# Kernel tuning notes

Measured on AMD Instinct MI355X. Metric: run time of the kernel, lower is better.

Reference implementation:

```python
import jax, jax.numpy as jnp
import numpy as np

EPS = 1e-5
KS = 3  # deformable kernel size
K2 = KS * KS


def conv2d(x, w, stride=1, padding=1):
    return jax.lax.conv_general_dilated(
        x, w, window_strides=(stride, stride),
        padding=[(padding, padding), (padding, padding)],
        dimension_numbers=("NCHW", "OIHW", "NCHW"))


def batchnorm(x, gamma, beta):
    # training-mode BN: batch statistics over (N, H, W)
    mean = jnp.mean(x, axis=(0, 2, 3), keepdims=True)
    var = jnp.var(x, axis=(0, 2, 3), keepdims=True)
    xhat = (x - mean) * jax.lax.rsqrt(var + EPS)
    return xhat * gamma[None, :, None, None] + beta[None, :, None, None]


def deform_conv(x, offsets, w, pad=1):
    # x: (B,C,H,W); offsets: (B,2*K2,H,W) -> first K2 channels = row (y)
    # offsets, next K2 = col (x) offsets; w: (O,C,KS,KS)
    B, C, H, W = x.shape
    xp = jnp.pad(x, ((0, 0), (0, 0), (pad, pad), (pad, pad)))
    Hp, Wp = H + 2 * pad, W + 2 * pad
    # base grid (center of each output pixel in padded coords)
    p0_y = jnp.arange(H, dtype=x.dtype) + pad            # (H,)
    p0_x = jnp.arange(W, dtype=x.dtype) + pad            # (W,)
    # kernel tap offsets in [-1, 0, 1]^2, row-major
    pn = jnp.stack(jnp.meshgrid(jnp.arange(KS) - pad, jnp.arange(KS) - pad,
                                indexing="ij"), axis=-1).reshape(K2, 2).astype(x.dtype)
    off = offsets.reshape(B, 2, K2, H, W)
    off_y = jnp.transpose(off[:, 0], (0, 2, 3, 1))       # (B,H,W,K2)
    off_x = jnp.transpose(off[:, 1], (0, 2, 3, 1))
    py = p0_y[None, :, None, None] + pn[:, 0][None, None, None, :] + off_y
    px = p0_x[None, None, :, None] + pn[:, 1][None, None, None, :] + off_x
    py = jnp.clip(py, 0.0, Hp - 1.0)
    px = jnp.clip(px, 0.0, Wp - 1.0)
    y0 = jnp.floor(py).astype(jnp.int32)
    x0 = jnp.floor(px).astype(jnp.int32)
    y1 = jnp.minimum(y0 + 1, Hp - 1)
    x1 = jnp.minimum(x0 + 1, Wp - 1)
    wy = (py - y0.astype(x.dtype))[:, None]              # (B,1,H,W,K2)
    wx = (px - x0.astype(x.dtype))[:, None]

    def gather(xb, yi, xi):                              # xb (C,Hp,Wp)
        return xb[:, yi, xi]                             # (C,H,W,K2)
    g = jax.vmap(gather)
    v00 = g(xp, y0, x0)
    v01 = g(xp, y0, x1)
    v10 = g(xp, y1, x0)
    v11 = g(xp, y1, x1)
    sampled = (v00 * (1 - wy) * (1 - wx) + v01 * (1 - wy) * wx +
               v10 * wy * (1 - wx) + v11 * wy * wx)      # (B,C,H,W,K2)
    return jnp.einsum("bchwk,ock->bohw", sampled, w.reshape(w.shape[0], C, K2))


def setup_inputs() -> dict:
    key = jax.random.key(0)
    ks = jax.random.split(key, 16)
    B, Cin, P, H, W = 64, 64, 64, 64, 64
    s = lambda k, shp, fan: jax.random.normal(k, shp, jnp.float32) * (fan ** -0.5)
    return {
        "x": jax.random.normal(ks[0], (B, Cin, H, W), jnp.float32),
        "conv1_w": s(ks[1], (P, Cin, 3, 3), Cin * 9),
        "bn1_g": jnp.ones((P,), jnp.float32), "bn1_b": jnp.zeros((P,), jnp.float32),
        "conv2_w": s(ks[2], (16, P, 1, 1), P),
        "bn2_g": jnp.ones((16,), jnp.float32), "bn2_b": jnp.zeros((16,), jnp.float32),
        "off_w": s(ks[3], (18, 16, 3, 3), 16 * 9) * 0.1,
        "off_b": jnp.zeros((18,), jnp.float32),
        "conv3_w": s(ks[4], (16, 16, 3, 3), 16 * 9),
        "bn3_g": jnp.ones((16,), jnp.float32), "bn3_b": jnp.zeros((16,), jnp.float32),
        "conv4_w": s(ks[5], (P, 16, 3, 3), 16 * 9),
        "bn4_g": jnp.ones((P,), jnp.float32), "bn4_b": jnp.zeros((P,), jnp.float32),
    }


def reference(x, conv1_w, bn1_g, bn1_b, conv2_w, bn2_g, bn2_b, off_w, off_b,
              conv3_w, bn3_g, bn3_b, conv4_w, bn4_g, bn4_b):
    out = jax.nn.relu(batchnorm(conv2d(x, conv1_w, 1, 1), bn1_g, bn1_b))
    out = jax.nn.relu(batchnorm(conv2d(out, conv2_w, 1, 0), bn2_g, bn2_b))
    offsets = conv2d(out, off_w, 1, 1) + off_b[None, :, None, None]
    out = jax.nn.relu(batchnorm(deform_conv(out, offsets, conv3_w), bn3_g, bn3_b))
    out = batchnorm(conv2d(out, conv4_w, 1, 1), bn4_g, bn4_b)
    out = out + x  # identity shortcut (stride=1, in_planes==planes)
    return jax.nn.relu(out)
```

## Files before the change

### kernel.cpp

```cpp
#include <hip/hip_runtime.h>

#define BN_N 262144.0f

typedef unsigned short u16;
typedef __attribute__((ext_vector_type(8))) short short8;
typedef __attribute__((ext_vector_type(4))) float floatx4;

#define RP1 4224
#define IS1 278784
#define RP2 1584
#define IS2 104544
#define H2P_TOTAL 6690816

static __device__ __forceinline__ u16 f2bf(float f) {
  union { float f; unsigned u; } v; v.f = f;
  unsigned u = v.u;
  return (u16)((u + 0x7FFFu + ((u >> 16) & 1u)) >> 16);
}
static __device__ __forceinline__ float bf2f(u16 h) {
  union { unsigned u; float f; } v; v.u = ((unsigned)h) << 16;
  return v.f;
}
static __device__ __forceinline__ void cp16(const u16* g, u16* l) {
  __builtin_amdgcn_global_load_lds((const __attribute__((address_space(1))) unsigned int*)g,
                                   (__attribute__((address_space(3))) unsigned int*)l, 16, 0, 0);
}

__global__ __launch_bounds__(256) void prep_weights_k(const float* __restrict__ w1,
                                                      const float* __restrict__ w4,
                                                      const float* __restrict__ w3,
                                                      const float* __restrict__ ow,
                                                      u16* __restrict__ Bsw, u16* __restrict__ Bsw4,
                                                      u16* __restrict__ Bsw3, u16* __restrict__ BswO) {
  int blk = blockIdx.x, tid = threadIdx.x;
  if (blk < 144) {
    int d = blk * 256 + tid;
    int kin = d & 7, n = (d >> 3) & 63, kgrp = (d >> 9) & 3, kc = d >> 11;
    int k = kc * 32 + kgrp * 8 + kin;
    int tap = k >> 6, c = k & 63;
    Bsw[d] = f2bf(w1[n * 576 + c * 9 + tap]);
  } else if (blk < 184) {
    int d = (blk - 144) * 256 + tid;
    int kin = d & 7, n = (d >> 3) & 63, lkk = (d >> 9) & 3, kk = d >> 11;
    int tap = kk * 2 + (lkk >> 1);
    int c = ((lkk & 1) << 3) + kin;
    float v = (tap < 9) ? w4[n * 144 + c * 9 + tap] : 0.f;
    Bsw4[d] = f2bf(v);
  } else if (blk < 194) {
    int d = (blk - 184) * 256 + tid;
    int kin = d & 7, n = (d >> 3) & 15, lkk = (d >> 7) & 3, kk = d >> 9;
    int k = kk * 32 + lkk * 8 + kin;
    int tap = k >> 4, c = k & 15;
    float v = (tap < 9) ? w3[n * 144 + c * 9 + tap] : 0.f;
    Bsw3[d] = f2bf(v);
  } else {
    int d = (blk - 194) * 256 + tid;
    int kin = d & 7, n = (d >> 3) & 31, lkk = (d >> 8) & 3, kk = d >> 10;
    int tap = kk * 2 + (lkk >> 1);
    int c = ((lkk & 1) << 3) + kin;
    float v = (tap < 9 && n < 18) ? ow[n * 144 + c * 9 + tap] : 0.f;
    BswO[d] = f2bf(v);
  }
}

__global__ __launch_bounds__(256) void prep_x_k(const float* __restrict__ x,
                                                u16* __restrict__ xp) {
  int yp = blockIdx.x;
  int b = blockIdx.y;
  int tid = threadIdx.x;
  u16* rowbase = xp + (size_t)(b * 66 + yp) * RP1;
  if (yp == 0 || yp == 65) {
    for (int i = tid; i < RP1 / 4; i += 256)
      ((ushort4*)rowbase)[i] = make_ushort4(0, 0, 0, 0);
    return;
  }
  int y = yp - 1;
  __shared__ __align__(16) u16 s[64][72];
  for (int i = tid; i < 4096; i += 256) {
    int c = i >> 6, xx = i & 63;
    s[xx][c] = f2bf(x[((b * 64 + c) << 12) + (y << 6) + xx]);
  }
  if (tid < 128) {
    int c = tid & 63;
    int pxp = (tid >> 6) ? 65 : 0;
    rowbase[pxp * 64 + c] = 0;
  }
  __syncthreads();
  for (int j = tid; j < 512; j += 256) {
    int xx = j >> 3, chunk = j & 7;
    int pxp = xx + 1;
    int ph = chunk ^ (pxp & 7);
    *(short8*)(rowbase + pxp * 64 + ph * 8) = *(const short8*)(&s[xx][chunk * 8]);
  }
}

__global__ __launch_bounds__(512, 2) void conv1_mfma(const u16* __restrict__ xp,
                                                     const u16* __restrict__ Bsw,
                                                     u16* __restrict__ h1,
                                                     float* __restrict__ sum1, float* __restrict__ sq1) {
  __shared__ __align__(16) u16 ring[43520];
  __shared__ float LS[256], LQ[256];
  const int tid = threadIdx.x;
  const int w8 = tid >> 6, l = tid & 63;
  const int r = w8 & 3, g = w8 >> 2;
  const int lm = l & 15, lk = l >> 4;
  const int b = blockIdx.x >> 2;
  const int quarter = blockIdx.x & 3;
  const int c0 = quarter * 8;
  const u16* xb = xp + (size_t)b * 66 * RP1;

  short8 bReg[18][2];
#pragma unroll
  for (int kk = 0; kk < 18; ++kk)
#pragma unroll
    for (int j = 0; j < 2; ++j)
      bReg[kk][j] = *(const short8*)(Bsw + (((kk * 4 + lk) * 64) + (g * 2 + j) * 16 + lm) * 8);

#pragma unroll
  for (int c = 0; c < 3; ++c) {
    const u16* src = xb + (size_t)(2 * (c0 + c)) * RP1;
    u16* dst = ring + ((c0 + c) % 5) * 8704;
    for (int s = w8; s < 17; s += 8) cp16(src + s * 512 + l * 8, dst + s * 512);
  }
  asm volatile("s_waitcnt vmcnt(0)" ::: "memory");
  __builtin_amdgcn_s_barrier();
  __builtin_amdgcn_sched_barrier(0);

  float ssum[2] = {0.f, 0.f}, sqsm[2] = {0.f, 0.f};

#pragma unroll 1
  for (int j = 0; j < 4; ++j) {
    const int y0 = quarter * 16 + j * 4;
    if (j < 3) {
#pragma unroll
      for (int c = 0; c < 2; ++c) {
        const int ch = c0 + 2 * j + 3 + c;
        const u16* src = xb + (size_t)(2 * ch) * RP1;
        u16* dst = ring + (ch % 5) * 8704;
        for (int s = w8; s < 17; s += 8) cp16(src + s * 512 + l * 8, dst + s * 512);
      }
      __builtin_amdgcn_sched_barrier(0);
    }

    floatx4 acc[4][2];
#pragma unroll
    for (int mt = 0; mt < 4; ++mt)
#pragma unroll
      for (int nb = 0; nb < 2; ++nb)
        acc[mt][nb] = (floatx4){0.f, 0.f, 0.f, 0.f};

#pragma unroll
    for (int kk = 0; kk < 18; ++kk) {
      const int tap = kk >> 1;
      const int dy = (tap < 3) ? 0 : ((tap < 6) ? 1 : 2);
      const int dx = tap - dy * 3;
      const int chunk16 = ((kk & 1) << 2) + lk;
      const int pr = y0 + r + dy;
      const u16* abase = ring + ((pr >> 1) % 5) * 8704 + (pr & 1) * 4224;
      short8 aF[4];
#pragma unroll
      for (int mt = 0; mt < 4; ++mt) {
        int pxp = mt * 16 + lm + dx;
        int ph = chunk16 ^ (pxp & 7);
        aF[mt] = *(const short8*)(abase + pxp * 64 + ph * 8);
      }
#pragma unroll
      for (int mt = 0; mt < 4; ++mt)
#pragma unroll
        for (int nb = 0; nb < 2; ++nb)
          acc[mt][nb] = __builtin_amdgcn_mfma_f32_16x16x32_bf16(aF[mt], bReg[kk][nb], acc[mt][nb], 0, 0, 0);
    }

    const int y = y0 + r;
#pragma unroll
    for (int mt = 0; mt < 4; ++mt)
#pragma unroll
      for (int nb = 0; nb < 2; ++nb) {
        const int oc = g * 32 + nb * 16 + lm;
        u16* dst = h1 + ((size_t)(b * 64 + oc) << 12) + (y << 6) + mt * 16 + (lk << 2);
        floatx4 v = acc[mt][nb];
        *(ushort4*)dst = make_ushort4(f2bf(v.x), f2bf(v.y), f2bf(v.z), f2bf(v.w));
      }

#pragma unroll
    for (int nb = 0; nb < 2; ++nb)
#pragma unroll
      for (int mt = 0; mt < 4; ++mt) {
        floatx4 a = acc[mt][nb];
        ssum[nb] += a.x + a.y + a.z + a.w;
        sqsm[nb] += a.x * a.x + a.y * a.y + a.z * a.z + a.w * a.w;
      }

    if (j < 3) {
      asm volatile("s_waitcnt vmcnt(8)" ::: "memory");
      __builtin_amdgcn_s_barrier();
      __builtin_amdgcn_sched_barrier(0);
    }
  }

#pragma unroll
  for (int nb = 0; nb < 2; ++nb) {
    ssum[nb] += __shfl_xor(ssum[nb], 16, 64);  ssum[nb] += __shfl_xor(ssum[nb], 32, 64);
    sqsm[nb] += __shfl_xor(sqsm[nb], 16, 64);  sqsm[nb] += __shfl_xor(sqsm[nb], 32, 64);
  }
  if (lk == 0) {
#pragma unroll
    for (int nb = 0; nb < 2; ++nb) {
      const int oc = g * 32 + nb * 16 + lm;
      LS[r * 64 + oc] = ssum[nb];  LQ[r * 64 + oc] = sqsm[nb];
    }
  }
  __syncthreads();
  if (tid < 64) atomicAdd(&sum1[tid], LS[tid] + LS[64 + tid] + LS[128 + tid] + LS[192 + tid]);
  else if (tid < 128) { int o = tid - 64; atomicAdd(&sq1[o], LQ[o] + LQ[64 + o] + LQ[128 + o] + LQ[192 + o]); }
}

__global__ __launch_bounds__(256) void conv2_k(const u16* __restrict__ h1,
                                               const float* __restrict__ w2,
                                               const float* __restrict__ sum1, const float* __restrict__ sq1,
                                               const float* __restrict__ g1, const float* __restrict__ b1,
                                               float* __restrict__ out,
                                               float* __restrict__ sum2, float* __restrict__ sq2) {
  __shared__ float s_wt[64 * 16];
  __shared__ float s_scale[64], s_shift[64];
  __shared__ float ls[4][16], lsq[4][16];
  int tid = threadIdx.x;
  for (int i = tid; i < 1024; i += 256) {
    int o = i >> 6, c = i & 63;
    s_wt[c * 16 + o] = w2[i];
  }
  if (tid < 64) {
    float m = sum1[tid] / BN_N;
    float var = sq1[tid] / BN_N - m * m;
    float sc = g1[tid] * rsqrtf(var + 1e-5f);
    s_scale[tid] = sc;
    s_shift[tid] = b1[tid] - m * sc;
  }
  __syncthreads();
  int p = blockIdx.x * 256 + tid;
  int b = p >> 12, r = p & 4095;
  const u16* src = h1 + ((size_t)b << 18) + r;
  float acc[16];
#pragma unroll
  for (int o = 0; o < 16; ++o) acc[o] = 0.f;
  for (int c = 0; c < 64; ++c) {
    float v = bf2f(src[c << 12]);
    v = fmaxf(v * s_scale[c] + s_shift[c], 0.f);
    const float* wp = &s_wt[c * 16];
    float4 w0 = *(const float4*)wp;
    float4 w1 = *(const float4*)(wp + 4);
    float4 w2v = *(const float4*)(wp + 8);
    float4 w3v = *(const float4*)(wp + 12);
    acc[0] += w0.x * v;  acc[1] += w0.y * v;  acc[2] += w0.z * v;  acc[3] += w0.w * v;
    acc[4] += w1.x * v;  acc[5] += w1.y * v;  acc[6] += w1.z * v;  acc[7] += w1.w * v;
    acc[8] += w2v.x * v; acc[9] += w2v.y * v; acc[10] += w2v.z * v; acc[11] += w2v.w * v;
    acc[12] += w3v.x * v; acc[13] += w3v.y * v; acc[14] += w3v.z * v; acc[15] += w3v.w * v;
  }
  float* dst = out + (size_t)p * 16;
#pragma unroll
  for (int c4 = 0; c4 < 4; ++c4)
    *(float4*)(dst + c4 * 4) = make_float4(acc[c4*4], acc[c4*4+1], acc[c4*4+2], acc[c4*4+3]);
  int lane = tid & 63, wv = tid >> 6;
#pragma unroll
  for (int o = 0; o < 16; ++o) {
    float s = acc[o], s2 = acc[o] * acc[o];
#pragma unroll
    for (int off = 32; off > 0; off >>= 1) {
      s += __shfl_down(s, off, 64);
      s2 += __shfl_down(s2, off, 64);
    }
    if (lane == 0) { ls[wv][o] = s; lsq[wv][o] = s2; }
  }
  __syncthreads();
  if (tid < 16) atomicAdd(&sum2[tid], ls[0][tid] + ls[1][tid] + ls[2][tid] + ls[3][tid]);
  else if (tid < 32) {
    int o = tid - 16;
    atomicAdd(&sq2[o], lsq[0][o] + lsq[1][o] + lsq[2][o] + lsq[3][o]);
  }
}

__global__ __launch_bounds__(256) void bnrelu2_k(const float* __restrict__ ws2,
                                                 const float* __restrict__ sum2, const float* __restrict__ sq2,
                                                 const float* __restrict__ g2, const float* __restrict__ b2,
                                                 u16* __restrict__ h2p) {
  __shared__ float s_scale[16], s_shift[16];
  int tid = threadIdx.x;
  if (tid < 16) {
    float m = sum2[tid] / BN_N;
    float var = sq2[tid] / BN_N - m * m;
    float sc = g2[tid] * rsqrtf(var + 1e-5f);
    s_scale[tid] = sc;
    s_shift[tid] = b2[tid] - m * sc;
  }
  __syncthreads();
  int p = blockIdx.x * 256 + tid;
  int b = p >> 12, r = p & 4095;
  int y = r >> 6, xx = r & 63;
  const float* src = ws2 + (size_t)p * 16;
  u16* dst = h2p + (size_t)(b * 66 + y + 1) * RP2 + (xx + 1) * 24;
#pragma unroll
  for (int c4 = 0; c4 < 4; ++c4) {
    float4 v = *(const float4*)(src + c4 * 4);
    u16 o0 = f2bf(fmaxf(v.x * s_scale[c4*4]   + s_shift[c4*4],   0.f));
    u16 o1 = f2bf(fmaxf(v.y * s_scale[c4*4+1] + s_shift[c4*4+1], 0.f));
    u16 o2 = f2bf(fmaxf(v.z * s_scale[c4*4+2] + s_shift[c4*4+2], 0.f));
    u16 o3 = f2bf(fmaxf(v.w * s_scale[c4*4+3] + s_shift[c4*4+3], 0.f));
    *(ushort4*)(dst + c4 * 4) = make_ushort4(o0, o1, o2, o3);
  }
}

__global__ __launch_bounds__(256) void offconv_mfma(const u16* __restrict__ h2p,
                                                    const u16* __restrict__ BswO,
                                                    const float* __restrict__ ob,
                                                    float* __restrict__ offs) {
  __shared__ __align__(16) u16 lA[9728];
  __shared__ __align__(16) u16 lB[5120];
  const int tid = threadIdx.x;
  const int w = tid >> 6, l = tid & 63;
  const int lm = l & 15, lk = l >> 4;
  const int b = blockIdx.x >> 4;
  const int y0 = (blockIdx.x & 15) << 2;
  const int y = y0 + w;
  const u16* src = h2p + ((size_t)b * 66 + y0) * RP2;
  for (int seg = w; seg < 19; seg += 4) cp16(src + seg * 512 + l * 8, lA + seg * 512);
  for (int seg = w; seg < 10; seg += 4) cp16(BswO + seg * 512 + l * 8, lB + seg * 512);
  __syncthreads();

  floatx4 acc[4][2];
#pragma unroll
  for (int mt = 0; mt < 4; ++mt)
#pragma unroll
    for (int nb = 0; nb < 2; ++nb)
      acc[mt][nb] = (floatx4){0.f, 0.f, 0.f, 0.f};

#pragma unroll
  for (int kk = 0; kk < 5; ++kk) {
    int tap = kk * 2 + (lk >> 1);
    if (tap > 8) tap = 8;
    const int dy = tap / 3, dx = tap - dy * 3;
    const int c0 = (lk & 1) << 3;
    const int rowoff = (w + dy) * RP2;
    short8 aF[4], bF[2];
#pragma unroll
    for (int mt = 0; mt < 4; ++mt)
      aF[mt] = *(const short8*)(lA + rowoff + (mt * 16 + lm + dx) * 24 + c0);
    const u16* bp = lB + (((kk * 4 + lk) * 32) + lm) * 8;
    bF[0] = *(const short8*)(bp);
    bF[1] = *(const short8*)(bp + 128);
#pragma unroll
    for (int mt = 0; mt < 4; ++mt)
#pragma unroll
      for (int nb = 0; nb < 2; ++nb)
        acc[mt][nb] = __builtin_amdgcn_mfma_f32_16x16x32_bf16(aF[mt], bF[nb], acc[mt][nb], 0, 0, 0);
  }

#pragma unroll
  for (int mt = 0; mt < 4; ++mt)
#pragma unroll
    for (int nb = 0; nb < 2; ++nb) {
      int oc = nb * 16 + lm;
      if (oc < 18) {
        float bias = ob[oc];
        floatx4 v = acc[mt][nb];
        v.x += bias; v.y += bias; v.z += bias; v.w += bias;
        float* dst = offs + (size_t)b * 73728 + (oc << 12) + (y << 6) + mt * 16 + (lk << 2);
        *(floatx4*)dst = v;
      }
    }
}

__global__ __launch_bounds__(256) void deform_mfma(const u16* __restrict__ h2p,
                                                   const float* __restrict__ offs,
                                                   const u16* __restrict__ Bsw3,
                                                   float* __restrict__ out,
                                                   float* __restrict__ sum3, float* __restrict__ sq3) {
  const int tid = threadIdx.x;
  const int w = tid >> 6, l = tid & 63;
  const int lm = l & 15, lk = l >> 4;
  const int pbase = blockIdx.x * 256 + w * 64;
  const int b = pbase >> 12;
  const u16* img = h2p + (size_t)b * IS2;
  const float* offp = offs + (size_t)b * 73728;

  short8 bf[5];
#pragma unroll
  for (int kk = 0; kk < 5; ++kk)
    bf[kk] = *(const short8*)(Bsw3 + (((kk * 4 + lk) * 16) + lm) * 8);

  floatx4 acc[4];
#pragma unroll
  for (int mt = 0; mt < 4; ++mt) acc[mt] = (floatx4){0.f, 0.f, 0.f, 0.f};

#pragma unroll
  for (int mt = 0; mt < 4; ++mt) {
    const int p = pbase + mt * 16 + lm;
    const int r = p & 4095;
    const int y = r >> 6, x = r & 63;
#pragma unroll
    for (int kk = 0; kk < 5; ++kk) {
      const int k0 = kk * 32 + lk * 8;
      int tap = k0 >> 4;
      const int c0 = k0 & 15;
      if (tap > 8) tap = 8;
      const int dy = tap / 3, dx = tap - dy * 3;
      float offy = offp[(tap << 12) + r];
      float offx = offp[((tap + 9) << 12) + r];
      float py = (float)(y + dy) + offy;
      float px = (float)(x + dx) + offx;
      py = fminf(fmaxf(py, 0.f), 65.f);
      px = fminf(fmaxf(px, 0.f), 65.f);
      float y0f = floorf(py), x0f = floorf(px);
      int y0 = (int)y0f, x0 = (int)x0f;
      int y1 = min(y0 + 1, 65), x1 = min(x0 + 1, 65);
      float wy = py - y0f, wx = px - x0f;
      float w00 = (1.f - wy) * (1.f - wx), w01 = (1.f - wy) * wx;
      float w10 = wy * (1.f - wx),         w11 = wy * wx;
      short8 v00 = *(const short8*)(img + (y0 * 66 + x0) * 24 + c0);
      short8 v01 = *(const short8*)(img + (y0 * 66 + x1) * 24 + c0);
      short8 v10 = *(const short8*)(img + (y1 * 66 + x0) * 24 + c0);
      short8 v11 = *(const short8*)(img + (y1 * 66 + x1) * 24 + c0);
      short8 a;
#pragma unroll
      for (int j = 0; j < 8; ++j) {
        float s = bf2f((u16)v00[j]) * w00 + bf2f((u16)v01[j]) * w01
                + bf2f((u16)v10[j]) * w10 + bf2f((u16)v11[j]) * w11;
        a[j] = (short)f2bf(s);
      }
      acc[mt] = __builtin_amdgcn_mfma_f32_16x16x32_bf16(a, bf[kk], acc[mt], 0, 0, 0);
    }
  }

  float s = 0.f, s2 = 0.f;
#pragma unroll
  for (int mt = 0; mt < 4; ++mt) {
    floatx4 a = acc[mt];
    s += a.x + a.y + a.z + a.w;
    s2 += a.x * a.x + a.y * a.y + a.z * a.z + a.w * a.w;
#pragma unroll
    for (int reg = 0; reg < 4; ++reg) {
      int pp = pbase + mt * 16 + lk * 4 + reg;
      out[(size_t)pp * 16 + lm] = acc[mt][reg];
    }
  }
  __shared__ float ls[4][16], lsq[4][16];
  s += __shfl_xor(s, 16, 64);  s += __shfl_xor(s, 32, 64);
  s2 += __shfl_xor(s2, 16, 64); s2 += __shfl_xor(s2, 32, 64);
  if (lk == 0) { ls[w][lm] = s; lsq[w][lm] = s2; }
  __syncthreads();
  if (tid < 16) atomicAdd(&sum3[tid], ls[0][tid] + ls[1][tid] + ls[2][tid] + ls[3][tid]);
  else if (tid < 32) {
    int o = tid - 16;
    atomicAdd(&sq3[o], lsq[0][o] + lsq[1][o] + lsq[2][o] + lsq[3][o]);
  }
}

__global__ __launch_bounds__(256) void bnrelu3_k(const float* __restrict__ wsd,
                                                 const float* __restrict__ sum3, const float* __restrict__ sq3,
                                                 const float* __restrict__ g3, const float* __restrict__ b3,
                                                 u16* __restrict__ h3p) {
  __shared__ float s_scale[16], s_shift[16];
  int tid = threadIdx.x;
  if (tid < 16) {
    float m = sum3[tid] / BN_N;
    float var = sq3[tid] / BN_N - m * m;
    float sc = g3[tid] * rsqrtf(var + 1e-5f);
    s_scale[tid] = sc;
    s_shift[tid] = b3[tid] - m * sc;
  }
  __syncthreads();
  int p = blockIdx.x * 256 + tid;
  int b = p >> 12, r = p & 4095;
  int y = r >> 6, xx = r & 63;
  const float* src = wsd + (size_t)p * 16;
  u16* dst = h3p + (size_t)(b * 66 + y + 1) * RP2 + (xx + 1) * 24;
#pragma unroll
  for (int c4 = 0; c4 < 4; ++c4) {
    float4 v = *(const float4*)(src + c4 * 4);
    u16 o0 = f2bf(fmaxf(v.x * s_scale[c4*4]   + s_shift[c4*4],   0.f));
    u16 o1 = f2bf(fmaxf(v.y * s_scale[c4*4+1] + s_shift[c4*4+1], 0.f));
    u16 o2 = f2bf(fmaxf(v.z * s_scale[c4*4+2] + s_shift[c4*4+2], 0.f));
    u16 o3 = f2bf(fmaxf(v.w * s_scale[c4*4+3] + s_shift[c4*4+3], 0.f));
    *(ushort4*)(dst + c4 * 4) = make_ushort4(o0, o1, o2, o3);
  }
}

__global__ __launch_bounds__(256) void conv4_mfma(const u16* __restrict__ h3p,
                                                  const u16* __restrict__ Bsw4,
                                                  u16* __restrict__ h4,
                                                  float* __restrict__ sum4, float* __restrict__ sq4) {
  __shared__ __align__(16) u16 lA[9728];
  __shared__ __align__(16) u16 lB[10240];
  const int tid = threadIdx.x;
  const int w = tid >> 6, l = tid & 63;
  const int lm = l & 15, lk = l >> 4;
  const int b = blockIdx.x >> 4;
  const int y0 = (blockIdx.x & 15) << 2;
  const int y = y0 + w;
  const u16* src = h3p + ((size_t)b * 66 + y0) * RP2;
  for (int seg = w; seg < 19; seg += 4) cp16(src + seg * 512 + l * 8, lA + seg * 512);
  for (int seg = w; seg < 20; seg += 4) cp16(Bsw4 + seg * 512 + l * 8, lB + seg * 512);
  __syncthreads();

  floatx4 acc[4][4];
#pragma unroll
  for (int mt = 0; mt < 4; ++mt)
#pragma unroll
    for (int nb = 0; nb < 4; ++nb)
      acc[mt][nb] = (floatx4){0.f, 0.f, 0.f, 0.f};

#pragma unroll
  for (int kk = 0; kk < 5; ++kk) {
    int tap = kk * 2 + (lk >> 1);
    if (tap > 8) tap = 8;
    const int dy = tap / 3, dx = tap - dy * 3;
    const int c0 = (lk & 1) << 3;
    const int rowoff = (w + dy) * RP2;
    short8 aF[4], bF[4];
#pragma unroll
    for (int mt = 0; mt < 4; ++mt)
      aF[mt] = *(const short8*)(lA + rowoff + (mt * 16 + lm + dx) * 24 + c0);
    const u16* bp = lB + (((kk * 4 + lk) * 64) + lm) * 8;
    bF[0] = *(const short8*)(bp);
    bF[1] = *(const short8*)(bp + 128);
    bF[2] = *(const short8*)(bp + 256);
    bF[3] = *(const short8*)(bp + 384);
#pragma unroll
    for (int mt = 0; mt < 4; ++mt)
#pragma unroll
      for (int nb = 0; nb < 4; ++nb)
        acc[mt][nb] = __builtin_amdgcn_mfma_f32_16x16x32_bf16(aF[mt], bF[nb], acc[mt][nb], 0, 0, 0);
  }

#pragma unroll
  for (int mt = 0; mt < 4; ++mt)
#pragma unroll
    for (int nb = 0; nb < 4; ++nb) {
      u16* dst = h4 + ((size_t)(b * 64 + nb * 16 + lm) << 12) + (y << 6) + mt * 16 + (lk << 2);
      floatx4 v = acc[mt][nb];
      *(ushort4*)dst = make_ushort4(f2bf(v.x), f2bf(v.y), f2bf(v.z), f2bf(v.w));
    }

  __syncthreads();
  float* LS = (float*)lA;
  float* LQ = LS + 256;
  float s[4], s2[4];
#pragma unroll
  for (int nb = 0; nb < 4; ++nb) {
    s[nb] = 0.f; s2[nb] = 0.f;
#pragma unroll
    for (int mt = 0; mt < 4; ++mt) {
      floatx4 a = acc[mt][nb];
      s[nb] += a.x + a.y + a.z + a.w;
      s2[nb] += a.x * a.x + a.y * a.y + a.z * a.z + a.w * a.w;
    }
    s[nb] += __shfl_xor(s[nb], 16, 64);  s[nb] += __shfl_xor(s[nb], 32, 64);
    s2[nb] += __shfl_xor(s2[nb], 16, 64); s2[nb] += __shfl_xor(s2[nb], 32, 64);
  }
  if (lk == 0) {
#pragma unroll
    for (int nb = 0; nb < 4; ++nb) { LS[w * 64 + nb * 16 + lm] = s[nb]; LQ[w * 64 + nb * 16 + lm] = s2[nb]; }
  }
  __syncthreads();
  if (tid < 64) atomicAdd(&sum4[tid], LS[tid] + LS[64 + tid] + LS[128 + tid] + LS[192 + tid]);
  else if (tid < 128) { int o = tid - 64; atomicAdd(&sq4[o], LQ[o] + LQ[64 + o] + LQ[128 + o] + LQ[192 + o]); }
}

__global__ __launch_bounds__(256) void final_k(const u16* __restrict__ h4,
                                               float* __restrict__ out,
                                               const float* __restrict__ x,
                                               const float* __restrict__ sum4, const float* __restrict__ sq4,
                                               const float* __restrict__ g4, const float* __restrict__ b4) {
  __shared__ float s_scale[64], s_shift[64];
  int tid = threadIdx.x;
  if (tid < 64) {
    float m = sum4[tid] / BN_N;
    float var = sq4[tid] / BN_N - m * m;
    float sc = g4[tid] * rsqrtf(var + 1e-5f);
    s_scale[tid] = sc;
    s_shift[tid] = b4[tid] - m * sc;
  }
  __syncthreads();
  int i = (blockIdx.x * 256 + tid) * 4;
  int c = (i >> 12) & 63;
  ushort4 q = *(const ushort4*)(h4 + i);
  float4 xv = *(const float4*)(x + i);
  float sc = s_scale[c], sh = s_shift[c];
  float4 v;
  v.x = fmaxf(bf2f(q.x) * sc + sh + xv.x, 0.f);
  v.y = fmaxf(bf2f(q.y) * sc + sh + xv.y, 0.f);
  v.z = fmaxf(bf2f(q.z) * sc + sh + xv.z, 0.f);
  v.w = fmaxf(bf2f(q.w) * sc + sh + xv.w, 0.f);
  *(float4*)(out + i) = v;
}

extern "C" void kernel_launch(void* const* d_in, const int* in_sizes, int n_in,
                              void* d_out, int out_size, void* d_ws, size_t ws_size,
                              hipStream_t stream) {
  const float* x  = (const float*)d_in[0];
  const float* w1 = (const float*)d_in[1];
  const float* g1 = (const float*)d_in[2];
  const float* b1 = (const float*)d_in[3];
  const float* w2 = (const float*)d_in[4];
  const float* g2 = (const float*)d_in[5];
  const float* b2 = (const float*)d_in[6];
  const float* ow = (const float*)d_in[7];
  const float* ob = (const float*)d_in[8];
  const float* w3 = (const float*)d_in[9];
  const float* g3 = (const float*)d_in[10];
  const float* b3 = (const float*)d_in[11];
  const float* w4 = (const float*)d_in[12];
  const float* g4 = (const float*)d_in[13];
  const float* b4 = (const float*)d_in[14];
  float* out = (float*)d_out;
  float* ws = (float*)d_ws;

  float* offs = ws;
  float* wsd  = offs + 4718592;
  float* ws2  = wsd + 4194304;
  float* h2pf = ws2 + 4194304;
  float* stats = h2pf + 4460544;
  float* sum1 = stats, *sq1 = stats + 64;
  float* sum2 = stats + 128, *sq2 = stats + 144;
  float* sum3 = stats + 160, *sq3 = stats + 176;
  float* sum4 = stats + 192, *sq4 = stats + 256;
  u16* xp   = (u16*)ws;
  u16* Bsw  = (u16*)(stats + 320);
  u16* Bsw4 = Bsw + 36864;
  u16* Bsw3 = Bsw4 + 10240;
  u16* BswO = Bsw3 + 2560;
  u16* h2p  = (u16*)h2pf;
  u16* h4   = (u16*)offs;
  u16* h1   = (u16*)out;

  hipMemsetAsync(stats, 0, 320 * sizeof(float), stream);
  hipMemsetAsync(h2p, 0, (size_t)H2P_TOTAL * sizeof(u16), stream);

  prep_weights_k<<<214, 256, 0, stream>>>(w1, w4, w3, ow, Bsw, Bsw4, Bsw3, BswO);
  prep_x_k<<<dim3(66, 64), 256, 0, stream>>>(x, xp);
  conv1_mfma<<<256, 512, 0, stream>>>(xp, Bsw, h1, sum1, sq1);
  conv2_k<<<1024, 256, 0, stream>>>(h1, w2, sum1, sq1, g1, b1, ws2, sum2, sq2);
  bnrelu2_k<<<1024, 256, 0, stream>>>(ws2, sum2, sq2, g2, b2, h2p);
  offconv_mfma<<<1024, 256, 0, stream>>>(h2p, BswO, ob, offs);
  deform_mfma<<<1024, 256, 0, stream>>>(h2p, offs, Bsw3, wsd, sum3, sq3);
  bnrelu3_k<<<1024, 256, 0, stream>>>(wsd, sum3, sq3, g3, b3, h2p );
  conv4_mfma<<<1024, 256, 0, stream>>>(h2p, Bsw4, h4, sum4, sq4);
  final_k<<<16384, 256, 0, stream>>>(h4, out, x, sum4, sq4, g4, b4);
}
```

Measured before the change: 317.1 us.

## Fuse offset conv into deformable conv and store intermediates as bf16

Merges the offset-prediction conv and the deformable conv into one kernel. Offsets are passed through shared memory instead of a global fp32 buffer, which removes one launch and the offset write and read. The conv2 and deform pre-BN intermediates are now stored as bf16 instead of fp32, halving that traffic. In exchange, BN statistics are still computed in fp32, but the stored pre-BN values lose precision. The fused kernel also uses more shared memory per block, which may lower occupancy.

New measurement: 308.5 us. 2.7% less time.

```diff
diff --git a/kernel.cpp b/kernel.cpp
--- a/kernel.cpp
+++ b/kernel.cpp
@@ -219,7 +219,7 @@
                                                const float* __restrict__ w2,
                                                const float* __restrict__ sum1, const float* __restrict__ sq1,
                                                const float* __restrict__ g1, const float* __restrict__ b1,
-                                               float* __restrict__ out,
+                                               u16* __restrict__ out,
                                                float* __restrict__ sum2, float* __restrict__ sq2) {
   __shared__ float s_wt[64 * 16];
   __shared__ float s_scale[64], s_shift[64];
@@ -256,10 +256,15 @@
     acc[8] += w2v.x * v; acc[9] += w2v.y * v; acc[10] += w2v.z * v; acc[11] += w2v.w * v;
     acc[12] += w3v.x * v; acc[13] += w3v.y * v; acc[14] += w3v.z * v; acc[15] += w3v.w * v;
   }
-  float* dst = out + (size_t)p * 16;
-#pragma unroll
-  for (int c4 = 0; c4 < 4; ++c4)
-    *(float4*)(dst + c4 * 4) = make_float4(acc[c4*4], acc[c4*4+1], acc[c4*4+2], acc[c4*4+3]);
+  u16* dst = out + (size_t)p * 16;
+  short8 o0, o1;
+#pragma unroll
+  for (int j = 0; j < 8; ++j) {
+    o0[j] = (short)f2bf(acc[j]);
+    o1[j] = (short)f2bf(acc[8 + j]);
+  }
+  *(short8*)(dst) = o0;
+  *(short8*)(dst + 8) = o1;
   int lane = tid & 63, wv = tid >> 6;
 #pragma unroll
   for (int o = 0; o < 16; ++o) {
@@ -279,7 +284,7 @@
   }
 }
 
-__global__ __launch_bounds__(256) void bnrelu2_k(const float* __restrict__ ws2,
+__global__ __launch_bounds__(256) void bnrelu2_k(const u16* __restrict__ ws2,
                                                  const float* __restrict__ sum2, const float* __restrict__ sq2,
                                                  const float* __restrict__ g2, const float* __restrict__ b2,
                                                  u16* __restrict__ h2p) {
@@ -296,25 +301,30 @@
   int p = blockIdx.x * 256 + tid;
   int b = p >> 12, r = p & 4095;
   int y = r >> 6, xx = r & 63;
-  const float* src = ws2 + (size_t)p * 16;
+  const u16* src = ws2 + (size_t)p * 16;
+  short8 v0 = *(const short8*)(src);
+  short8 v1 = *(const short8*)(src + 8);
   u16* dst = h2p + (size_t)(b * 66 + y + 1) * RP2 + (xx + 1) * 24;
-#pragma unroll
-  for (int c4 = 0; c4 < 4; ++c4) {
-    float4 v = *(const float4*)(src + c4 * 4);
-    u16 o0 = f2bf(fmaxf(v.x * s_scale[c4*4]   + s_shift[c4*4],   0.f));
-    u16 o1 = f2bf(fmaxf(v.y * s_scale[c4*4+1] + s_shift[c4*4+1], 0.f));
-    u16 o2 = f2bf(fmaxf(v.z * s_scale[c4*4+2] + s_shift[c4*4+2], 0.f));
-    u16 o3 = f2bf(fmaxf(v.w * s_scale[c4*4+3] + s_shift[c4*4+3], 0.f));
-    *(ushort4*)(dst + c4 * 4) = make_ushort4(o0, o1, o2, o3);
-  }
-}
-
-__global__ __launch_bounds__(256) void offconv_mfma(const u16* __restrict__ h2p,
-                                                    const u16* __restrict__ BswO,
-                                                    const float* __restrict__ ob,
-                                                    float* __restrict__ offs) {
+  short8 o0, o1;
+#pragma unroll
+  for (int j = 0; j < 8; ++j) {
+    o0[j] = (short)f2bf(fmaxf(bf2f((u16)v0[j]) * s_scale[j] + s_shift[j], 0.f));
+    o1[j] = (short)f2bf(fmaxf(bf2f((u16)v1[j]) * s_scale[j + 8] + s_shift[j + 8], 0.f));
+  }
+  *(short8*)(dst) = o0;
+  *(short8*)(dst + 8) = o1;
+}
+
+__global__ __launch_bounds__(256) void offdeform_mfma(const u16* __restrict__ h2p,
+                                                      const u16* __restrict__ BswO,
+                                                      const float* __restrict__ ob,
+                                                      const u16* __restrict__ Bsw3,
+                                                      u16* __restrict__ out,
+                                                      float* __restrict__ sum3, float* __restrict__ sq3) {
   __shared__ __align__(16) u16 lA[9728];
   __shared__ __align__(16) u16 lB[5120];
+  __shared__ float offsT[4][64][20];
+  __shared__ float ls[4][16], lsq[4][16];
   const int tid = threadIdx.x;
   const int w = tid >> 6, l = tid & 63;
   const int lm = l & 15, lk = l >> 4;
@@ -362,40 +372,26 @@
       if (oc < 18) {
         float bias = ob[oc];
         floatx4 v = acc[mt][nb];
-        v.x += bias; v.y += bias; v.z += bias; v.w += bias;
-        float* dst = offs + (size_t)b * 73728 + (oc << 12) + (y << 6) + mt * 16 + (lk << 2);
-        *(floatx4*)dst = v;
+#pragma unroll
+        for (int reg = 0; reg < 4; ++reg)
+          offsT[w][mt * 16 + lk * 4 + reg][oc] = v[reg] + bias;
       }
     }
-}
-
-__global__ __launch_bounds__(256) void deform_mfma(const u16* __restrict__ h2p,
-                                                   const float* __restrict__ offs,
-                                                   const u16* __restrict__ Bsw3,
-                                                   float* __restrict__ out,
-                                                   float* __restrict__ sum3, float* __restrict__ sq3) {
-  const int tid = threadIdx.x;
-  const int w = tid >> 6, l = tid & 63;
-  const int lm = l & 15, lk = l >> 4;
-  const int pbase = blockIdx.x * 256 + w * 64;
-  const int b = pbase >> 12;
+  __syncthreads();
+
   const u16* img = h2p + (size_t)b * IS2;
-  const float* offp = offs + (size_t)b * 73728;
-
   short8 bf[5];
 #pragma unroll
   for (int kk = 0; kk < 5; ++kk)
     bf[kk] = *(const short8*)(Bsw3 + (((kk * 4 + lk) * 16) + lm) * 8);
 
-  floatx4 acc[4];
-#pragma unroll
-  for (int mt = 0; mt < 4; ++mt) acc[mt] = (floatx4){0.f, 0.f, 0.f, 0.f};
+  floatx4 accd[4];
+#pragma unroll
+  for (int mt = 0; mt < 4; ++mt) accd[mt] = (floatx4){0.f, 0.f, 0.f, 0.f};
 
 #pragma unroll
   for (int mt = 0; mt < 4; ++mt) {
-    const int p = pbase + mt * 16 + lm;
-    const int r = p & 4095;
-    const int y = r >> 6, x = r & 63;
+    const int x = mt * 16 + lm;
 #pragma unroll
     for (int kk = 0; kk < 5; ++kk) {
       const int k0 = kk * 32 + lk * 8;
@@ -403,46 +399,46 @@
       const int c0 = k0 & 15;
       if (tap > 8) tap = 8;
       const int dy = tap / 3, dx = tap - dy * 3;
-      float offy = offp[(tap << 12) + r];
-      float offx = offp[((tap + 9) << 12) + r];
+      float offy = offsT[w][x][tap];
+      float offx = offsT[w][x][tap + 9];
       float py = (float)(y + dy) + offy;
       float px = (float)(x + dx) + offx;
       py = fminf(fmaxf(py, 0.f), 65.f);
       px = fminf(fmaxf(px, 0.f), 65.f);
       float y0f = floorf(py), x0f = floorf(px);
-      int y0 = (int)y0f, x0 = (int)x0f;
-      int y1 = min(y0 + 1, 65), x1 = min(x0 + 1, 65);
+      int yy0 = (int)y0f, xx0 = (int)x0f;
+      int yy1 = min(yy0 + 1, 65), xx1 = min(xx0 + 1, 65);
       float wy = py - y0f, wx = px - x0f;
       float w00 = (1.f - wy) * (1.f - wx), w01 = (1.f - wy) * wx;
       float w10 = wy * (1.f - wx),         w11 = wy * wx;
-      short8 v00 = *(const short8*)(img + (y0 * 66 + x0) * 24 + c0);
-      short8 v01 = *(const short8*)(img + (y0 * 66 + x1) * 24 + c0);
-      short8 v10 = *(const short8*)(img + (y1 * 66 + x0) * 24 + c0);
-      short8 v11 = *(const short8*)(img + (y1 * 66 + x1) * 24 + c0);
+      short8 v00 = *(const short8*)(img + (yy0 * 66 + xx0) * 24 + c0);
+      short8 v01 = *(const short8*)(img + (yy0 * 66 + xx1) * 24 + c0);
+      short8 v10 = *(const short8*)(img + (yy1 * 66 + xx0) * 24 + c0);
+      short8 v11 = *(const short8*)(img + (yy1 * 66 + xx1) * 24 + c0);
       short8 a;
 #pragma unroll
-      for (int j = 0; j < 8; ++j) {
-        float s = bf2f((u16)v00[j]) * w00 + bf2f((u16)v01[j]) * w01
-                + bf2f((u16)v10[j]) * w10 + bf2f((u16)v11[j]) * w11;
-        a[j] = (short)f2bf(s);
+      for (int jj = 0; jj < 8; ++jj) {
+        float s = bf2f((u16)v00[jj]) * w00 + bf2f((u16)v01[jj]) * w01
+                + bf2f((u16)v10[jj]) * w10 + bf2f((u16)v11[jj]) * w11;
+        a[jj] = (short)f2bf(s);
       }
-      acc[mt] = __builtin_amdgcn_mfma_f32_16x16x32_bf16(a, bf[kk], acc[mt], 0, 0, 0);
-    }
-  }
-
+      accd[mt] = __builtin_amdgcn_mfma_f32_16x16x32_bf16(a, bf[kk], accd[mt], 0, 0, 0);
+    }
+  }
+
+  const int pbase = (b << 12) + (y << 6);
   float s = 0.f, s2 = 0.f;
 #pragma unroll
   for (int mt = 0; mt < 4; ++mt) {
-    floatx4 a = acc[mt];
+    floatx4 a = accd[mt];
     s += a.x + a.y + a.z + a.w;
     s2 += a.x * a.x + a.y * a.y + a.z * a.z + a.w * a.w;
 #pragma unroll
     for (int reg = 0; reg < 4; ++reg) {
       int pp = pbase + mt * 16 + lk * 4 + reg;
-      out[(size_t)pp * 16 + lm] = acc[mt][reg];
-    }
-  }
-  __shared__ float ls[4][16], lsq[4][16];
+      out[(size_t)pp * 16 + lm] = f2bf(a[reg]);
+    }
+  }
   s += __shfl_xor(s, 16, 64);  s += __shfl_xor(s, 32, 64);
   s2 += __shfl_xor(s2, 16, 64); s2 += __shfl_xor(s2, 32, 64);
   if (lk == 0) { ls[w][lm] = s; lsq[w][lm] = s2; }
@@ -454,7 +450,7 @@
   }
 }
 
-__global__ __launch_bounds__(256) void bnrelu3_k(const float* __restrict__ wsd,
+__global__ __launch_bounds__(256) void bnrelu3_k(const u16* __restrict__ wsd,
                                                  const float* __restrict__ sum3, const float* __restrict__ sq3,
                                                  const float* __restrict__ g3, const float* __restrict__ b3,
                                                  u16* __restrict__ h3p) {
@@ -471,17 +467,18 @@
   int p = blockIdx.x * 256 + tid;
   int b = p >> 12, r = p & 4095;
   int y = r >> 6, xx = r & 63;
-  const float* src = wsd + (size_t)p * 16;
+  const u16* src = wsd + (size_t)p * 16;
+  short8 v0 = *(const short8*)(src);
+  short8 v1 = *(const short8*)(src + 8);
   u16* dst = h3p + (size_t)(b * 66 + y + 1) * RP2 + (xx + 1) * 24;
-#pragma unroll
-  for (int c4 = 0; c4 < 4; ++c4) {
-    float4 v = *(const float4*)(src + c4 * 4);
-    u16 o0 = f2bf(fmaxf(v.x * s_scale[c4*4]   + s_shift[c4*4],   0.f));
-    u16 o1 = f2bf(fmaxf(v.y * s_scale[c4*4+1] + s_shift[c4*4+1], 0.f));
-    u16 o2 = f2bf(fmaxf(v.z * s_scale[c4*4+2] + s_shift[c4*4+2], 0.f));
-    u16 o3 = f2bf(fmaxf(v.w * s_scale[c4*4+3] + s_shift[c4*4+3], 0.f));
-    *(ushort4*)(dst + c4 * 4) = make_ushort4(o0, o1, o2, o3);
-  }
+  short8 o0, o1;
+#pragma unroll
+  for (int j = 0; j < 8; ++j) {
+    o0[j] = (short)f2bf(fmaxf(bf2f((u16)v0[j]) * s_scale[j] + s_shift[j], 0.f));
+    o1[j] = (short)f2bf(fmaxf(bf2f((u16)v1[j]) * s_scale[j + 8] + s_shift[j + 8], 0.f));
+  }
+  *(short8*)(dst) = o0;
+  *(short8*)(dst + 8) = o1;
 }
 
 __global__ __launch_bounds__(256) void conv4_mfma(const u16* __restrict__ h3p,
@@ -614,8 +611,8 @@
   float* out = (float*)d_out;
   float* ws = (float*)d_ws;
 
-  float* offs = ws;
-  float* wsd  = offs + 4718592;
+  float* reg0 = ws;
+  float* wsd  = reg0 + 4718592;
   float* ws2  = wsd + 4194304;
   float* h2pf = ws2 + 4194304;
   float* stats = h2pf + 4460544;
@@ -629,8 +626,10 @@
   u16* Bsw3 = Bsw4 + 10240;
   u16* BswO = Bsw3 + 2560;
   u16* h2p  = (u16*)h2pf;
-  u16* h4   = (u16*)offs;
+  u16* h4   = (u16*)reg0;
   u16* h1   = (u16*)out;
+  u16* ws2b = (u16*)ws2;
+  u16* wsdb = (u16*)wsd;
 
   hipMemsetAsync(stats, 0, 320 * sizeof(float), stream);
   hipMemsetAsync(h2p, 0, (size_t)H2P_TOTAL * sizeof(u16), stream);
@@ -638,11 +637,10 @@
   prep_weights_k<<<214, 256, 0, stream>>>(w1, w4, w3, ow, Bsw, Bsw4, Bsw3, BswO);
   prep_x_k<<<dim3(66, 64), 256, 0, stream>>>(x, xp);
   conv1_mfma<<<256, 512, 0, stream>>>(xp, Bsw, h1, sum1, sq1);
-  conv2_k<<<1024, 256, 0, stream>>>(h1, w2, sum1, sq1, g1, b1, ws2, sum2, sq2);
-  bnrelu2_k<<<1024, 256, 0, stream>>>(ws2, sum2, sq2, g2, b2, h2p);
-  offconv_mfma<<<1024, 256, 0, stream>>>(h2p, BswO, ob, offs);
-  deform_mfma<<<1024, 256, 0, stream>>>(h2p, offs, Bsw3, wsd, sum3, sq3);
-  bnrelu3_k<<<1024, 256, 0, stream>>>(wsd, sum3, sq3, g3, b3, h2p );
+  conv2_k<<<1024, 256, 0, stream>>>(h1, w2, sum1, sq1, g1, b1, ws2b, sum2, sq2);
+  bnrelu2_k<<<1024, 256, 0, stream>>>(ws2b, sum2, sq2, g2, b2, h2p);
+  offdeform_mfma<<<1024, 256, 0, stream>>>(h2p, BswO, ob, Bsw3, wsdb, sum3, sq3);
+  bnrelu3_k<<<1024, 256, 0, stream>>>(wsdb, sum3, sq3, g3, b3, h2p );
   conv4_mfma<<<1024, 256, 0, stream>>>(h2p, Bsw4, h4, sum4, sq4);
   final_k<<<16384, 256, 0, stream>>>(h4, out, x, sum4, sq4, g4, b4);
 }
```
